# Performance work log

Hardware: AMD Instinct MI355X
Metric: run time of the kernel (lower is better)

Reference implementation:

```python
import jax, jax.numpy as jnp
import numpy as np

# PyramidAttention (core of UrbanODE): channel=64, reduction=2, ksize=3, level=5,
# stride=1, softmax_scale=10, average=True, res_scale=1, input 32x32.
SCALES = [1.0, 0.9, 0.8, 0.7, 0.6]
SOFTMAX_SCALE = 10.0
ESCAPE_NAN = 1e-4


def _prelu(x, a):
    return jnp.where(x >= 0, x, a * x)


def _conv1x1(x, w, b):
    # x: [B,Cin,H,W], w: [Cout,Cin], b: [Cout]
    return jnp.einsum('oc,bchw->bohw', w, x) + b[None, :, None, None]


def _resize_nearest(x, s):
    # torch F.interpolate(mode='nearest', recompute_scale_factor=True):
    # out = floor(in*s), src_idx = floor(dst*in/out)
    H, W = x.shape[2], x.shape[3]
    oh, ow = int(np.floor(H * s)), int(np.floor(W * s))
    iy = (np.arange(oh) * H) // oh
    ix = (np.arange(ow) * W) // ow
    return x[:, :, iy][:, :, :, ix]


def _patches3(x):
    # 3x3 patches, stride 1, 'same' (pad 1): [B,C,H,W] -> [B,H*W,C,3,3]
    # flatten order matches torch Unfold: (C, kh, kw)
    B, C, H, W = x.shape
    xp = jnp.pad(x, ((0, 0), (0, 0), (1, 1), (1, 1)))
    cols = jnp.stack([xp[:, :, dy:dy + H, dx:dx + W]
                      for dy in range(3) for dx in range(3)], axis=2)  # [B,C,9,H,W]
    return cols.reshape(B, C, 3, 3, H * W).transpose(0, 4, 1, 2, 3)


def _tconv_fold(yi, raw_w):
    # per-sample conv_transpose2d(yi, raw_w, stride=1, padding=1)
    # yi: [N,H,W], raw_w: [N,C,3,3] -> out [C,H,W]
    # transpose-conv (s=1,p=1) == SAME correlation with spatially-flipped kernel
    k = jnp.flip(raw_w, (-2, -1)).transpose(1, 0, 2, 3)  # [C,N,3,3]
    return jax.lax.conv_general_dilated(
        yi[None], k, (1, 1), ((1, 1), (1, 1)),
        dimension_numbers=('NCHW', 'OIHW', 'NCHW'))[0]


def setup_inputs() -> dict:
    key = jax.random.key(0)
    ks = jax.random.split(key, 8)
    B, C, H, W = 32, 64, 32, 32
    C2 = C // 2
    return {
        'x': jax.random.normal(ks[0], (B, C, H, W), jnp.float32),
        'w_base': 0.05 * jax.random.normal(ks[1], (C2, C), jnp.float32),
        'b_base': jnp.zeros((C2,), jnp.float32),
        'a_base': jnp.full((1,), 0.25, jnp.float32),
        'w_match': 0.05 * jax.random.normal(ks[2], (C2, C), jnp.float32),
        'b_match': jnp.zeros((C2,), jnp.float32),
        'a_match': jnp.full((1,), 0.25, jnp.float32),
        'w_asm': 0.05 * jax.random.normal(ks[3], (C, C), jnp.float32),
        'b_asm': jnp.zeros((C,), jnp.float32),
        'a_asm': jnp.full((1,), 0.25, jnp.float32),
    }


def reference(x, w_base, b_base, a_base, w_match, b_match, a_match,
              w_asm, b_asm, a_asm):
    B, C, H, W = x.shape
    match_base = _prelu(_conv1x1(x, w_base, b_base), a_base)  # [B,C/2,H,W]

    wi_list, raw_list = [], []
    for s in SCALES:
        ref = x if s == 1.0 else _resize_nearest(x, s)
        base = _prelu(_conv1x1(ref, w_asm, b_asm), a_asm)      # [B,C,h,w]
        raw_list.append(_patches3(base))                        # [B,hw,C,3,3]
        refm = _prelu(_conv1x1(ref, w_match, b_match), a_match)  # [B,C/2,h,w]
        wi_list.append(_patches3(refm))                         # [B,hw,C/2,3,3]
    wi = jnp.concatenate(wi_list, axis=1)        # [B,N,C/2,3,3], N=3278
    raw_w = jnp.concatenate(raw_list, axis=1)    # [B,N,C,3,3]

    # per-filter L2 normalization (escape_NaN)
    norm = jnp.sqrt(jnp.sum(wi * wi, axis=(2, 3, 4), keepdims=True))
    wi_n = wi / jnp.maximum(norm, ESCAPE_NAN)

    # correlation of query patches with dynamic filters: batched GEMM
    N = wi.shape[1]
    xp = _patches3(match_base).reshape(B, H * W, -1)   # [B,HW,C/2*9]
    yi = jnp.einsum('bnk,bpk->bnp', wi_n.reshape(B, N, -1), xp)  # [B,N,HW]
    yi = jax.nn.softmax(yi * SOFTMAX_SCALE, axis=1)
    yi = yi.reshape(B, N, H, W)

    out = jax.vmap(_tconv_fold)(yi, raw_w) / 4.0       # [B,C,H,W]
    return out + x  # res_scale = 1
```

## Files before the change

### kernel.cpp

```cpp
#include <hip/hip_runtime.h>
#include <hip/hip_bf16.h>
#include <math.h>

#define BB 32
#define CC 64
#define C2 32
#define HH 32
#define WW 32
#define HW 1024
#define NTOT 3278
#define NPAD2 3328
#define NT26 26
#define NT64 52

typedef __bf16   bf16x8 __attribute__((ext_vector_type(8)));
typedef _Float16 half8  __attribute__((ext_vector_type(8)));
typedef float    f32x4  __attribute__((ext_vector_type(4)));

__device__ __constant__ int SC_SIZE[5] = {32, 28, 25, 22, 19};
__device__ __constant__ int SC_OFF[6]  = {0, 1024, 1808, 2433, 2917, 3278};

#define XS_STR 65
#define WS_STR 132
__global__ void __launch_bounds__(256, 1) k_feats(
        const float* __restrict__ x,
        const float* __restrict__ wb, const float* __restrict__ bb, const float* __restrict__ ab,
        const float* __restrict__ wm, const float* __restrict__ bm, const float* __restrict__ am,
        const float* __restrict__ wa, const float* __restrict__ ba, const float* __restrict__ aa,
        _Float16* __restrict__ mft, _Float16* __restrict__ rft,
        __bf16* __restrict__ basef,
        float* __restrict__ mbss, float* __restrict__ rmss) {
    __shared__ float Xs[64 * XS_STR];
    __shared__ float Wls[64 * WS_STR];
    __shared__ float bsh[128];
    __shared__ float ash3[3];
    int tid = threadIdx.x;
    int g0 = blockIdx.x * 64;
    int b = g0 >> 10, p0 = g0 & 1023;

    const float* xb = x + (size_t)b * CC * HW + p0;
    for (int i = tid; i < 64 * 64; i += 256) {
        int c = i >> 6, p = i & 63;
        Xs[c * XS_STR + p] = xb[(size_t)c * HW + p];
    }
    for (int i = tid; i < 128 * 64; i += 256) {
        int o = i >> 6, c = i & 63;
        float w = (o < 32) ? wb[o * CC + c] : (o < 64) ? wm[(o - 32) * CC + c] : wa[(o - 64) * CC + c];
        Wls[c * WS_STR + o] = w;
    }
    if (tid < 128) bsh[tid] = (tid < 32) ? bb[tid] : (tid < 64) ? bm[tid - 32] : ba[tid - 64];
    if (tid == 128) ash3[0] = ab[0];
    if (tid == 129) ash3[1] = am[0];
    if (tid == 130) ash3[2] = aa[0];
    __syncthreads();

    int p = tid & 63, og = tid >> 6;
    int o0 = og * 32;
    float acc[32];
#pragma unroll
    for (int oi = 0; oi < 32; ++oi) acc[oi] = bsh[o0 + oi];
    for (int c = 0; c < 64; ++c) {
        float xv = Xs[c * XS_STR + p];
        const float* wr = &Wls[c * WS_STR + o0];
#pragma unroll
        for (int oi = 0; oi < 32; ++oi) acc[oi] += wr[oi] * xv;
    }
    int pp = p0 + p;
    if (og < 2) {
        float alpha = ash3[og], ss = 0.f;
        half8 hv[4];
#pragma unroll
        for (int oi = 0; oi < 32; ++oi) {
            float v = acc[oi] >= 0.f ? acc[oi] : alpha * acc[oi];
            ss += v * v;
            hv[oi >> 3][oi & 7] = (_Float16)v;
        }
        _Float16* d = (og == 0 ? mft : rft) + ((size_t)b * HW + pp) * 32;
#pragma unroll
        for (int q = 0; q < 4; ++q) *(half8*)&d[q * 8] = hv[q];
        if (og == 0) mbss[(size_t)b * HW + pp] = ss;
        else         rmss[(size_t)b * HW + pp] = ss;
    } else {
        float alpha = ash3[2];
        int ob = o0 - 64;
#pragma unroll
        for (int oi = 0; oi < 32; ++oi) {
            float v = acc[oi] >= 0.f ? acc[oi] : alpha * acc[oi];
            basef[((size_t)b * CC + ob + oi) * HW + pp] = (__bf16)v;
        }
    }
}

__global__ void k_nbr(int* __restrict__ nbr_pos) {
    int n = blockIdx.x * blockDim.x + threadIdx.x;
    if (n >= NTOT) return;
    int s = 0;
    while (s < 4 && n >= SC_OFF[s + 1]) ++s;
    int q = n - SC_OFF[s];
    int hs = SC_SIZE[s];
    int ny = q / hs, nx = q % hs;
    for (int dy = 0; dy < 3; ++dy)
        for (int dx = 0; dx < 3; ++dx) {
            int yy = ny + dy - 1, xx = nx + dx - 1;
            int pos = -1;
            if (yy >= 0 && yy < hs && xx >= 0 && xx < hs)
                pos = ((yy * HH) / hs) * WW + (xx * WW) / hs;
            nbr_pos[(dy * 3 + dx) * NTOT + n] = pos;
        }
}

__global__ void k_qnorm(const float* __restrict__ mbss, float* __restrict__ qub) {
    int t = blockIdx.x * blockDim.x + threadIdx.x;
    int b = t >> 10, p = t & 1023;
    int y = p >> 5, x = p & 31;
    float s = 0.f;
#pragma unroll
    for (int dy = 0; dy < 3; ++dy)
#pragma unroll
        for (int dx = 0; dx < 3; ++dx) {
            int yy = y + dy - 1, xx = x + dx - 1;
            if (yy >= 0 && yy < HH && xx >= 0 && xx < WW)
                s += mbss[(size_t)b * HW + yy * WW + xx];
        }
    qub[t] = 10.0f * sqrtf(s);
}

__global__ void k_norms(const float* __restrict__ rmss, const int* __restrict__ nbr_pos,
                        float* __restrict__ sinv) {
    int t = blockIdx.x * blockDim.x + threadIdx.x;
    if (t >= BB * NTOT) return;
    int b = t / NTOT, n = t % NTOT;
    float sum = 0.f;
#pragma unroll
    for (int kk = 0; kk < 9; ++kk) {
        int pos = nbr_pos[kk * NTOT + n];
        if (pos >= 0) sum += rmss[(size_t)b * HW + pos];
    }
    sinv[t] = 10.0f / fmaxf(sqrtf(sum), 1e-4f);
}

__global__ void k_vgather(const __bf16* __restrict__ basef, const int* __restrict__ nbr_pos,
                          __bf16* __restrict__ Vb, int b0) {
    int c = blockIdx.x, cb = blockIdx.y;
    int tid = threadIdx.x;
    __shared__ __bf16 row[HW];
    const __bf16* src = basef + ((size_t)(b0 + cb) * CC + c) * HW;
    for (int i = tid; i < HW / 8; i += 256)
        *(bf16x8*)&row[i * 8] = *(const bf16x8*)&src[i * 8];
    __syncthreads();
    for (int t = tid; t < 9 * (NPAD2 / 8); t += 256) {
        int kk = t / (NPAD2 / 8), nq = t - kk * (NPAD2 / 8);
        int n0 = nq * 8;
        const int* nb = &nbr_pos[kk * NTOT];
        bf16x8 v8;
#pragma unroll
        for (int u = 0; u < 8; ++u) {
            int n = n0 + u;
            __bf16 v = (__bf16)0.f;
            if (n < NTOT) {
                int pos = nb[n];
                if (pos >= 0) v = row[pos];
            }
            v8[u] = v;
        }
        int m = c * 9 + kk;
        int nt = n0 >> 6;
        int j0s = (((n0 & 63) >> 3) ^ (m & 7)) << 3;
        *(bf16x8*)&Vb[(((size_t)cb * NT64 + nt) * 576 + m) * 64 + j0s] = v8;
    }
}

__global__ void __launch_bounds__(512) k_corr_mfma(
        const _Float16* __restrict__ mft, const _Float16* __restrict__ rft,
        const int* __restrict__ nbr_pos,
        const float* __restrict__ sinv, const float* __restrict__ qub,
        __bf16* __restrict__ tbuf, float* __restrict__ partS, int b0) {
    int ptile = blockIdx.x;
    int ntile = blockIdx.y;
    int cb    = blockIdx.z;
    int tid  = threadIdx.x;
    int lane = tid & 63, wave = tid >> 6;
    int row16 = lane & 15, quad = lane >> 4;
    int wrP = wave >> 2, wrN = wave & 3;
    int p0 = ptile * 128, n0 = ntile * 128;

    __shared__ _Float16 Ah[128 * 40];
    __shared__ _Float16 Bh[128 * 40];
    __shared__ short nbrs[9][128];
    __shared__ short posA[9][128];
    __shared__ float sMub[128];
    __shared__ float redS[8][64];
    __shared__ __bf16 Tls[8][16 * 36];

    if (tid < 128) sMub[tid] = qub[(size_t)(b0 + cb) * HW + p0 + tid];
    for (int i = tid; i < 9 * 128; i += 512) {
        int kk = i >> 7, j = i & 127;
        int n = n0 + j;
        nbrs[kk][j] = (short)((n < NTOT) ? nbr_pos[kk * NTOT + n] : -1);
        int pg = p0 + j;
        int py = (pg >> 5) + kk / 3 - 1, px = (pg & 31) + kk % 3 - 1;
        posA[kk][j] = (short)((py >= 0 && py < HH && px >= 0 && px < WW) ? (py * WW + px) : -1);
    }

    const _Float16* mh = mft + (size_t)(b0 + cb) * HW * 32;
    const _Float16* rh = rft + (size_t)(b0 + cb) * HW * 32;

    f32x4 acc[4][2];
#pragma unroll
    for (int i = 0; i < 4; ++i)
#pragma unroll
        for (int j = 0; j < 2; ++j) acc[i][j] = (f32x4){0.f, 0.f, 0.f, 0.f};

    half8 zero8;
#pragma unroll
    for (int u = 0; u < 8; ++u) zero8[u] = (_Float16)0.f;

    __syncthreads();

    half8 pA, pB;
    int ar = tid >> 2, ac = (tid & 3) * 8;
    auto gatherA = [&](int kk, half8* dst) {
        int pa = posA[kk][ar];
        *dst = (pa >= 0) ? *(const half8*)(mh + (size_t)pa * 32 + ac) : zero8;
    };
    auto gatherB = [&](int kk, half8* dst) {
        int pos = nbrs[kk][ar];
        *dst = (pos >= 0) ? *(const half8*)(rh + (size_t)pos * 32 + ac) : zero8;
    };

    gatherA(0, &pA);
    gatherB(0, &pB);

    for (int kk = 0; kk < 9; ++kk) {
        __syncthreads();
        *(half8*)&Ah[ar * 40 + ac] = pA;
        *(half8*)&Bh[ar * 40 + ac] = pB;
        if (kk < 8) {
            gatherA(kk + 1, &pA);
            gatherB(kk + 1, &pB);
        }
        __syncthreads();
        half8 af[4], bf[2];
#pragma unroll
        for (int m = 0; m < 4; ++m)
            af[m] = *(const half8*)&Ah[(wrP * 64 + m * 16 + row16) * 40 + quad * 8];
#pragma unroll
        for (int nb = 0; nb < 2; ++nb)
            bf[nb] = *(const half8*)&Bh[(wrN * 32 + nb * 16 + row16) * 40 + quad * 8];
#pragma unroll
        for (int m = 0; m < 4; ++m)
#pragma unroll
            for (int nb = 0; nb < 2; ++nb)
                acc[m][nb] = __builtin_amdgcn_mfma_f32_16x16x32_f16(af[m], bf[nb], acc[m][nb], 0, 0, 0);
    }

    int nn[2];
    float sv[2];
    bool valid[2];
#pragma unroll
    for (int nb = 0; nb < 2; ++nb) {
        nn[nb] = n0 + wrN * 32 + nb * 16 + row16;
        valid[nb] = nn[nb] < NTOT;
        sv[nb] = valid[nb] ? sinv[(size_t)(b0 + cb) * NTOT + nn[nb]] : 0.f;
    }
    float sm[4][4];
#pragma unroll
    for (int m = 0; m < 4; ++m)
#pragma unroll
        for (int r = 0; r < 4; ++r) sm[m][r] = 0.f;

    int tr = lane >> 2, tc = (lane & 3) * 8;
#pragma unroll
    for (int m = 0; m < 4; ++m) {
#pragma unroll
        for (int nb = 0; nb < 2; ++nb) {
#pragma unroll
            for (int r = 0; r < 4; ++r) {
                float mub = sMub[wrP * 64 + m * 16 + quad * 4 + r];
                float e = valid[nb] ? __expf(acc[m][nb][r] * sv[nb] - mub) : 0.f;
                Tls[wave][(quad * 4 + r) * 36 + nb * 16 + row16] = (__bf16)e;
                sm[m][r] += e;
            }
        }
        bf16x8 v = *(const bf16x8*)&Tls[wave][tr * 36 + tc];
        int nglob = n0 + wrN * 32 + tc;
        int nt = nglob >> 6, j0 = nglob & 63;
        int j0s = ((j0 >> 3) ^ (tr & 7)) << 3;
        int p = p0 + wrP * 64 + m * 16 + tr;
        *(bf16x8*)&tbuf[(((size_t)cb * NT64 + nt) * HW + p) * 64 + j0s] = v;
    }

#pragma unroll
    for (int msk = 1; msk < 16; msk <<= 1)
#pragma unroll
        for (int m = 0; m < 4; ++m)
#pragma unroll
            for (int r = 0; r < 4; ++r) sm[m][r] += __shfl_xor(sm[m][r], msk, 64);
    if (row16 == 0)
#pragma unroll
        for (int m = 0; m < 4; ++m)
#pragma unroll
            for (int r = 0; r < 4; ++r) redS[wave][m * 16 + quad * 4 + r] = sm[m][r];
    __syncthreads();
    if ((wave == 0 || wave == 4) && row16 == 0) {
#pragma unroll
        for (int m = 0; m < 4; ++m)
#pragma unroll
            for (int r = 0; r < 4; ++r) {
                int p = m * 16 + quad * 4 + r;
                float S = redS[wrP * 4 + 0][p] + redS[wrP * 4 + 1][p] +
                          redS[wrP * 4 + 2][p] + redS[wrP * 4 + 3][p];
                partS[((size_t)cb * HW + p0 + wrP * 64 + p) * NT26 + ntile] = S;
            }
    }
}

__global__ void k_rowsum(const float* __restrict__ partS, float* __restrict__ fin) {
    int row = blockIdx.x * 256 + threadIdx.x;
    float s = 0.f;
#pragma unroll
    for (int nt = 0; nt < NT26; ++nt) s += partS[(size_t)row * NT26 + nt];
    fin[row] = 1.0f / fmaxf(s, 1e-38f);
}

__device__ __forceinline__ void gload16(const void* g, void* l) {
    __builtin_amdgcn_global_load_lds(
        (const __attribute__((address_space(1))) void*)g,
        (__attribute__((address_space(3))) void*)l, 16, 0, 0);
}

#define A_KSTRIDE (576 * 64 * 2)
#define B_KSTRIDE (1024 * 64 * 2)
#define FM 192
#define FP 128

__global__ void __launch_bounds__(512, 4) k_fold_mfma(
        const __bf16* __restrict__ Vb, const __bf16* __restrict__ tbuf,
        const float* __restrict__ fin, __bf16* __restrict__ outacc) {
    int ptile = blockIdx.x;
    int mtile = blockIdx.y;
    int cb    = blockIdx.z;
    int tid  = threadIdx.x;
    int lane = tid & 63, wave = tid >> 6;
    int row16 = lane & 15, quad = lane >> 4;
    int wrM = wave >> 2, wrN = wave & 3;

    __shared__ __bf16 Als[2][FM * 64];
    __shared__ __bf16 Bls[2][FP * 64];

    const char* Ag = (const char*)(Vb   + (((size_t)cb * NT64) * 576  + (size_t)mtile * FM) * 64);
    const char* Bg = (const char*)(tbuf + (((size_t)cb * NT64) * 1024 + (size_t)ptile * FP) * 64);

    f32x4 acc[6][2];
#pragma unroll
    for (int i = 0; i < 6; ++i)
#pragma unroll
        for (int j = 0; j < 2; ++j) acc[i][j] = (f32x4){0.f, 0.f, 0.f, 0.f};

    int lo16 = lane * 16;
    auto stage = [&](int sb, int kt) {
#pragma unroll
        for (int i = 0; i < 5; ++i) {
            int q = wave * 5 + i;
            if (q < 24) {
                gload16(Ag + (size_t)kt * A_KSTRIDE + q * 1024 + lo16,
                        (char*)&Als[sb][0] + q * 1024);
            } else {
                gload16(Bg + (size_t)kt * B_KSTRIDE + (q - 24) * 1024 + lo16,
                        (char*)&Bls[sb][0] + (q - 24) * 1024);
            }
        }
    };

    int sg = row16 & 7;
    auto compute = [&](int sb) {
#pragma unroll
        for (int kh = 0; kh < 2; ++kh) {
            int ko = ((kh * 4 + quad) ^ sg) << 3;
            bf16x8 af[6], bf[2];
#pragma unroll
            for (int mb = 0; mb < 6; ++mb)
                af[mb] = *(const bf16x8*)&Als[sb][(wrM * 96 + mb * 16 + row16) * 64 + ko];
#pragma unroll
            for (int pbi = 0; pbi < 2; ++pbi)
                bf[pbi] = *(const bf16x8*)&Bls[sb][(wrN * 32 + pbi * 16 + row16) * 64 + ko];
#pragma unroll
            for (int mb = 0; mb < 6; ++mb)
#pragma unroll
                for (int pbi = 0; pbi < 2; ++pbi)
                    acc[mb][pbi] = __builtin_amdgcn_mfma_f32_16x16x32_bf16(af[mb], bf[pbi], acc[mb][pbi], 0, 0, 0);
        }
    };

    stage(0, 0);
    __syncthreads();
    int cur = 0;
    for (int kt = 0; kt < NT64; ++kt) {
        if (kt + 1 < NT64) stage(cur ^ 1, kt + 1);
        compute(cur);
        __syncthreads();
        cur ^= 1;
    }

    float fsc[2];
#pragma unroll
    for (int pbi = 0; pbi < 2; ++pbi)
        fsc[pbi] = fin[(size_t)cb * HW + ptile * FP + wrN * 32 + pbi * 16 + row16];
#pragma unroll
    for (int mb = 0; mb < 6; ++mb)
#pragma unroll
        for (int pbi = 0; pbi < 2; ++pbi) {
#pragma unroll
            for (int r = 0; r < 4; ++r) {
                int mg = mtile * FM + wrM * 96 + mb * 16 + quad * 4 + r;
                int pg = ptile * FP + wrN * 32 + pbi * 16 + row16;
                outacc[((size_t)cb * 576 + mg) * HW + pg] = (__bf16)(acc[mb][pbi][r] * fsc[pbi]);
            }
        }
}

__global__ void k_epilogue(const float* __restrict__ x, const __bf16* __restrict__ outacc,
                           float* __restrict__ out, int b0) {
    int t = blockIdx.x * blockDim.x + threadIdx.x;
    int cb = t >> 16;
    int c = (t >> 10) & 63;
    int p = t & 1023;
    int b = b0 + cb;
    int y = p >> 5, xx = p & 31;
    float acc = 0.f;
#pragma unroll
    for (int ky = 0; ky < 3; ++ky)
#pragma unroll
        for (int kx = 0; kx < 3; ++kx) {
            int py = y + 1 - ky, px = xx + 1 - kx;
            if (py >= 0 && py < HH && px >= 0 && px < WW)
                acc += (float)outacc[((size_t)cb * 576 + c * 9 + ky * 3 + kx) * HW + py * WW + px];
        }
    size_t o = ((size_t)b * CC + c) * HW + p;
    out[o] = x[o] + 0.25f * acc;
}

extern "C" void kernel_launch(void* const* d_in, const int* in_sizes, int n_in,
                              void* d_out, int out_size, void* d_ws, size_t ws_size,
                              hipStream_t stream) {
    const float* x       = (const float*)d_in[0];
    const float* w_base  = (const float*)d_in[1];
    const float* b_base  = (const float*)d_in[2];
    const float* a_base  = (const float*)d_in[3];
    const float* w_match = (const float*)d_in[4];
    const float* b_match = (const float*)d_in[5];
    const float* a_match = (const float*)d_in[6];
    const float* w_asm   = (const float*)d_in[7];
    const float* b_asm   = (const float*)d_in[8];
    const float* a_asm   = (const float*)d_in[9];
    float* out = (float*)d_out;

    const size_t fixed = ((size_t)BB * HW * 32 * 2) * 2 + ((size_t)BB * CC * HW * 2) +
                         ((size_t)BB * HW * 4) * 3 + ((size_t)BB * NTOT * 4) +
                         ((size_t)9 * NTOT * 4) + 65536;
    const size_t perCB = ((size_t)HW * NPAD2 * 2) + ((size_t)HW * NT26 * 4) +
                         ((size_t)HW * 4) + ((size_t)576 * NPAD2 * 2) +
                         ((size_t)576 * HW * 2) + 65536;
    int CB = 32;
    while (CB > 1 && fixed + perCB * CB > ws_size) CB >>= 1;

    char* ws = (char*)d_ws;
    size_t off = 0;
    auto alloc_b = [&](size_t bytes) {
        void* p = (void*)(ws + off);
        off += bytes;
        off = (off + 255) & ~(size_t)255;
        return p;
    };
    _Float16* mft   = (_Float16*)alloc_b((size_t)BB * HW * 32 * 2);
    _Float16* rft   = (_Float16*)alloc_b((size_t)BB * HW * 32 * 2);
    __bf16* base_f  = (__bf16*)alloc_b((size_t)BB * CC * HW * 2);
    float*  mbss    = (float*)alloc_b((size_t)BB * HW * 4);
    float*  rmss    = (float*)alloc_b((size_t)BB * HW * 4);
    float*  qub     = (float*)alloc_b((size_t)BB * HW * 4);
    float*  sinv    = (float*)alloc_b((size_t)BB * NTOT * 4);
    int*    nbr_pos = (int*)alloc_b((size_t)9 * NTOT * 4);
    __bf16* tbuf    = (__bf16*)alloc_b((size_t)CB * HW * NPAD2 * 2);
    float*  partS   = (float*)alloc_b((size_t)CB * HW * NT26 * 4);
    float*  fin     = (float*)alloc_b((size_t)CB * HW * 4);
    __bf16* Vb      = (__bf16*)alloc_b((size_t)CB * 576 * NPAD2 * 2);
    __bf16* outacc  = (__bf16*)alloc_b((size_t)CB * 576 * HW * 2);
    if (off > ws_size) return;

    k_feats<<<BB * HW / 64, 256, 0, stream>>>(
        x, w_base, b_base, a_base, w_match, b_match, a_match, w_asm, b_asm, a_asm,
        mft, rft, base_f, mbss, rmss);
    k_nbr<<<(NTOT + 255) / 256, 256, 0, stream>>>(nbr_pos);
    k_qnorm<<<BB * HW / 256, 256, 0, stream>>>(mbss, qub);
    k_norms<<<(BB * NTOT + 255) / 256, 256, 0, stream>>>(rmss, nbr_pos, sinv);

    for (int b0 = 0; b0 < BB; b0 += CB) {
        k_corr_mfma<<<dim3(8, NT26, CB), 512, 0, stream>>>(
            mft, rft, nbr_pos, sinv, qub, tbuf, partS, b0);
        k_rowsum<<<CB * HW / 256, 256, 0, stream>>>(partS, fin);
        k_vgather<<<dim3(CC, CB), 256, 0, stream>>>(base_f, nbr_pos, Vb, b0);
        k_fold_mfma<<<dim3(8, 3, CB), 512, 0, stream>>>(Vb, tbuf, fin, outacc);
        k_epilogue<<<CB * CC * HW / 256, 256, 0, stream>>>(x, outacc, out, b0);
    }
}
```

Before: 577.4 us.

## Double-buffer corr GEMM staging via direct global-to-LDS loads with swizzle

The correlation kernel's A/B tile staging now uses global_load_lds (16B per lane) straight into double-buffered LDS, with an XOR swizzle in place of row padding. Out-of-range neighbours point at a small zeroed pad buffer, which k_nbr initialises. The loop needs one barrier per k-step instead of two, and the next step's loads overlap the current MFMAs. In exchange it relies on the implicit LDS placement of global_load_lds (wave base + lane*16) matching the swizzle layout.

```diff
diff --git a/kernel.cpp b/kernel.cpp
--- a/kernel.cpp
+++ b/kernel.cpp
@@ -91,7 +91,8 @@
     }
 }
 
-__global__ void k_nbr(int* __restrict__ nbr_pos) {
+__global__ void k_nbr(int* __restrict__ nbr_pos, float* __restrict__ zpad) {
+    if (blockIdx.x == 0 && threadIdx.x < 64) zpad[threadIdx.x] = 0.f;
     int n = blockIdx.x * blockDim.x + threadIdx.x;
     if (n >= NTOT) return;
     int s = 0;
@@ -170,10 +171,17 @@
     }
 }
 
+__device__ __forceinline__ void gload16(const void* g, void* l) {
+    __builtin_amdgcn_global_load_lds(
+        (const __attribute__((address_space(1))) void*)g,
+        (__attribute__((address_space(3))) void*)l, 16, 0, 0);
+}
+
 __global__ void __launch_bounds__(512) k_corr_mfma(
         const _Float16* __restrict__ mft, const _Float16* __restrict__ rft,
         const int* __restrict__ nbr_pos,
         const float* __restrict__ sinv, const float* __restrict__ qub,
+        const float* __restrict__ zpad,
         __bf16* __restrict__ tbuf, float* __restrict__ partS, int b0) {
     int ptile = blockIdx.x;
     int ntile = blockIdx.y;
@@ -184,8 +192,8 @@
     int wrP = wave >> 2, wrN = wave & 3;
     int p0 = ptile * 128, n0 = ntile * 128;
 
-    __shared__ _Float16 Ah[128 * 40];
-    __shared__ _Float16 Bh[128 * 40];
+    __shared__ _Float16 Abuf[2][128 * 32];
+    __shared__ _Float16 Bbuf[2][128 * 32];
     __shared__ short nbrs[9][128];
     __shared__ short posA[9][128];
     __shared__ float sMub[128];
@@ -202,8 +210,9 @@
         posA[kk][j] = (short)((py >= 0 && py < HH && px >= 0 && px < WW) ? (py * WW + px) : -1);
     }
 
-    const _Float16* mh = mft + (size_t)(b0 + cb) * HW * 32;
-    const _Float16* rh = rft + (size_t)(b0 + cb) * HW * 32;
+    const char* mh = (const char*)(mft + (size_t)(b0 + cb) * HW * 32);
+    const char* rh = (const char*)(rft + (size_t)(b0 + cb) * HW * 32);
+    const char* zp = (const char*)zpad;
 
     f32x4 acc[4][2];
 #pragma unroll
@@ -211,47 +220,42 @@
 #pragma unroll
         for (int j = 0; j < 2; ++j) acc[i][j] = (f32x4){0.f, 0.f, 0.f, 0.f};
 
-    half8 zero8;
-#pragma unroll
-    for (int u = 0; u < 8; ++u) zero8[u] = (_Float16)0.f;
-
     __syncthreads();
 
-    half8 pA, pB;
-    int ar = tid >> 2, ac = (tid & 3) * 8;
-    auto gatherA = [&](int kk, half8* dst) {
-        int pa = posA[kk][ar];
-        *dst = (pa >= 0) ? *(const half8*)(mh + (size_t)pa * 32 + ac) : zero8;
+    int srow = wave * 16 + (lane >> 2);
+    int sshift = (((lane & 3) ^ (srow & 3)) << 4);
+    auto stageAB = [&](int sb, int kk) {
+        int pa = posA[kk][srow];
+        const char* sa = (pa >= 0) ? mh + (size_t)pa * 64 + sshift : zp;
+        gload16(sa, (char*)&Abuf[sb][0] + wave * 1024);
+        int pb = nbrs[kk][srow];
+        const char* sbp = (pb >= 0) ? rh + (size_t)pb * 64 + sshift : zp;
+        gload16(sbp, (char*)&Bbuf[sb][0] + wave * 1024);
     };
-    auto gatherB = [&](int kk, half8* dst) {
-        int pos = nbrs[kk][ar];
-        *dst = (pos >= 0) ? *(const half8*)(rh + (size_t)pos * 32 + ac) : zero8;
-    };
-
-    gatherA(0, &pA);
-    gatherB(0, &pB);
-
+
+    stageAB(0, 0);
+    __syncthreads();
+    int cur = 0;
     for (int kk = 0; kk < 9; ++kk) {
-        __syncthreads();
-        *(half8*)&Ah[ar * 40 + ac] = pA;
-        *(half8*)&Bh[ar * 40 + ac] = pB;
-        if (kk < 8) {
-            gatherA(kk + 1, &pA);
-            gatherB(kk + 1, &pB);
-        }
-        __syncthreads();
+        if (kk < 8) stageAB(cur ^ 1, kk + 1);
         half8 af[4], bf[2];
 #pragma unroll
-        for (int m = 0; m < 4; ++m)
-            af[m] = *(const half8*)&Ah[(wrP * 64 + m * 16 + row16) * 40 + quad * 8];
-#pragma unroll
-        for (int nb = 0; nb < 2; ++nb)
-            bf[nb] = *(const half8*)&Bh[(wrN * 32 + nb * 16 + row16) * 40 + quad * 8];
+        for (int m = 0; m < 4; ++m) {
+            int row = wrP * 64 + m * 16 + row16;
+            af[m] = *(const half8*)&Abuf[cur][row * 32 + ((quad ^ (row & 3)) << 3)];
+        }
+#pragma unroll
+        for (int nb = 0; nb < 2; ++nb) {
+            int row = wrN * 32 + nb * 16 + row16;
+            bf[nb] = *(const half8*)&Bbuf[cur][row * 32 + ((quad ^ (row & 3)) << 3)];
+        }
 #pragma unroll
         for (int m = 0; m < 4; ++m)
 #pragma unroll
             for (int nb = 0; nb < 2; ++nb)
                 acc[m][nb] = __builtin_amdgcn_mfma_f32_16x16x32_f16(af[m], bf[nb], acc[m][nb], 0, 0, 0);
+        __syncthreads();
+        cur ^= 1;
     }
 
     int nn[2];
@@ -321,12 +325,6 @@
 #pragma unroll
     for (int nt = 0; nt < NT26; ++nt) s += partS[(size_t)row * NT26 + nt];
     fin[row] = 1.0f / fmaxf(s, 1e-38f);
-}
-
-__device__ __forceinline__ void gload16(const void* g, void* l) {
-    __builtin_amdgcn_global_load_lds(
-        (const __attribute__((address_space(1))) void*)g,
-        (__attribute__((address_space(3))) void*)l, 16, 0, 0);
 }
 
 #define A_KSTRIDE (576 * 64 * 2)
@@ -480,6 +478,7 @@
     float*  qub     = (float*)alloc_b((size_t)BB * HW * 4);
     float*  sinv    = (float*)alloc_b((size_t)BB * NTOT * 4);
     int*    nbr_pos = (int*)alloc_b((size_t)9 * NTOT * 4);
+    float*  zpad    = (float*)alloc_b(256);
     __bf16* tbuf    = (__bf16*)alloc_b((size_t)CB * HW * NPAD2 * 2);
     float*  partS   = (float*)alloc_b((size_t)CB * HW * NT26 * 4);
     float*  fin     = (float*)alloc_b((size_t)CB * HW * 4);
@@ -490,13 +489,13 @@
     k_feats<<<BB * HW / 64, 256, 0, stream>>>(
         x, w_base, b_base, a_base, w_match, b_match, a_match, w_asm, b_asm, a_asm,
         mft, rft, base_f, mbss, rmss);
-    k_nbr<<<(NTOT + 255) / 256, 256, 0, stream>>>(nbr_pos);
+    k_nbr<<<(NTOT + 255) / 256, 256, 0, stream>>>(nbr_pos, zpad);
     k_qnorm<<<BB * HW / 256, 256, 0, stream>>>(mbss, qub);
     k_norms<<<(BB * NTOT + 255) / 256, 256, 0, stream>>>(rmss, nbr_pos, sinv);
 
     for (int b0 = 0; b0 < BB; b0 += CB) {
         k_corr_mfma<<<dim3(8, NT26, CB), 512, 0, stream>>>(
-            mft, rft, nbr_pos, sinv, qub, tbuf, partS, b0);
+            mft, rft, nbr_pos, sinv, qub, zpad, tbuf, partS, b0);
         k_rowsum<<<CB * HW / 256, 256, 0, stream>>>(partS, fin);
         k_vgather<<<dim3(CC, CB), 256, 0, stream>>>(base_f, nbr_pos, Vb, b0);
         k_fold_mfma<<<dim3(8, 3, CB), 512, 0, stream>>>(Vb, tbuf, fin, outacc);
```

New measurement: 554.7 us. 3.9% less time.
